# Optimization experiments

Hardware: AMD Instinct MI355X
Metric: run time of the kernel (lower is better)

## Reference

```python
import jax, jax.numpy as jnp
import numpy as np

N_NODES = 50000
N_EDGES = 1600000
N_GRAPHS = 64


def _gcn_conv(x, row, col, ew, W, b, n_nodes):
    # x: [N, Fin] -> [N, Fout]; PyG GCNConv: lin, add self-loops (w=1),
    # symmetric normalization, scatter-add at target (col), + bias.
    x = x @ W
    loop = jnp.arange(n_nodes, dtype=row.dtype)
    r = jnp.concatenate([row, loop])
    c = jnp.concatenate([col, loop])
    w = jnp.concatenate([ew, jnp.ones((n_nodes,), dtype=ew.dtype)])
    deg = jax.ops.segment_sum(w, c, num_segments=n_nodes)
    dinv = jnp.where(deg > 0, jax.lax.rsqrt(jnp.where(deg > 0, deg, 1.0)), 0.0)
    norm = dinv[r] * w * dinv[c]                      # [E+N]
    msg = x[r] * norm[:, None]                        # [E+N, Fout] (dominant traffic)
    out = jax.ops.segment_sum(msg, c, num_segments=n_nodes)
    return out + b


def setup_inputs() -> dict:
    key = jax.random.key(0)
    ks = jax.random.split(key, 12)
    x = jax.random.normal(ks[0], (N_NODES, 128), dtype=jnp.float32)
    edge_index = jax.random.randint(ks[1], (2, N_EDGES), 0, N_NODES, dtype=jnp.int32)
    edge_attr = jax.random.uniform(ks[2], (N_EDGES,), dtype=jnp.float32)
    batch = jnp.sort(jax.random.randint(ks[3], (N_NODES,), 0, N_GRAPHS, dtype=jnp.int32))
    glorot = lambda k, fi, fo: jax.random.normal(k, (fi, fo), jnp.float32) * np.sqrt(2.0 / (fi + fo))
    return {
        "x": x, "edge_index": edge_index, "edge_attr": edge_attr, "batch": batch,
        "W1": glorot(ks[4], 128, 128), "b1": jnp.zeros((128,), jnp.float32),
        "W2": glorot(ks[5], 128, 64), "b2": jnp.zeros((64,), jnp.float32),
        "fc1_W": glorot(ks[6], 64, 128), "fc1_b": jnp.zeros((128,), jnp.float32),
        "fc2_W": glorot(ks[7], 128, 2), "fc2_b": jnp.zeros((2,), jnp.float32),
    }


def reference(x, edge_index, edge_attr, batch, W1, b1, W2, b2, fc1_W, fc1_b, fc2_W, fc2_b):
    row, col = edge_index[0], edge_index[1]
    h = jax.nn.relu(_gcn_conv(x, row, col, edge_attr, W1, b1, N_NODES))
    x1 = jax.nn.relu(_gcn_conv(h, row, col, edge_attr, W2, b2, N_NODES))
    # global mean pool over batch ids
    sums = jax.ops.segment_sum(x1, batch, num_segments=N_GRAPHS)
    cnt = jax.ops.segment_sum(jnp.ones((N_NODES,), x1.dtype), batch, num_segments=N_GRAPHS)
    x2 = sums / jnp.maximum(cnt, 1.0)[:, None]        # [B, 64]
    # dropout is identity in eval mode
    h = jax.nn.relu(x2 @ fc1_W + fc1_b)
    logits = h @ fc2_W + fc2_b                        # [B, 2]
    return jax.nn.log_softmax(logits, axis=1)
```

## Files before the change

### kernel.cpp

```cpp
#include <hip/hip_runtime.h>
#include <hip/hip_bf16.h>


#define CAP 64
#define OVFCAP 8192
#define NRANGE 512
#define MAXNRP 2048
#define BSTR 68
#define KP 136
#define PARTNB 1024

typedef float v2f  __attribute__((ext_vector_type(2)));
typedef float f32x4 __attribute__((ext_vector_type(4)));
typedef short bf16x8 __attribute__((ext_vector_type(8)));

__device__ inline unsigned short f2bf(float f) {
    unsigned u = __float_as_uint(f);
    u += 0x7FFFu + ((u >> 16) & 1u);
    return (unsigned short)(u >> 16);
}
__device__ inline void fp8x4_to_f32(unsigned w, float* o) {
    v2f lo = __builtin_amdgcn_cvt_pk_f32_fp8((int)w, false);
    v2f hi = __builtin_amdgcn_cvt_pk_f32_fp8((int)w, true);
    o[0] = lo[0]; o[1] = lo[1]; o[2] = hi[0]; o[3] = hi[1];
}
__device__ inline unsigned f32x4_to_fp8(float a, float b, float c, float d) {
    int w = 0;
    w = __builtin_amdgcn_cvt_pk_fp8_f32(a, b, w, false);
    w = __builtin_amdgcn_cvt_pk_fp8_f32(c, d, w, true);
    return (unsigned)w;
}
__device__ inline float dinv_of(int ws) {
    return rsqrtf((float)ws * (1.0f / 32768.0f) + 1.0f);
}

__global__ void part_kernel(const int* __restrict__ rows, const int* __restrict__ cols,
                            const float* __restrict__ ew, int* __restrict__ rangeCnt,
                            uint2* __restrict__ rng, int E, int NR, int RSEG,
                            const float* __restrict__ W1, const float* __restrict__ W2,
                            unsigned short* __restrict__ wt1, unsigned short* __restrict__ wt2) {
    const int t = threadIdx.x;
    if (blockIdx.x >= PARTNB) {
        if (blockIdx.x == PARTNB) {
            for (int i = t; i < 128 * 128; i += 256) {
                int c = i >> 7, k = i & 127;
                wt1[c * KP + k] = f2bf(W1[k * 128 + c]);
            }
        } else {
            for (int i = t; i < 64 * 128; i += 256) {
                int c = i >> 7, k = i & 127;
                wt2[c * KP + k] = f2bf(W2[k * 64 + c]);
            }
        }
        return;
    }
    __shared__ int hc[NRANGE];
    const int CS = (E + PARTNB - 1) / PARTNB;
    const int e0 = blockIdx.x * CS, e1 = min(e0 + CS, E);
    for (int i = t; i < NRANGE; i += 256) hc[i] = 0;
    __syncthreads();
    for (int e = e0 + t; e < e1; e += 256) {
        int r = cols[e] / NR;
        atomicAdd(&hc[r], 1);
    }
    __syncthreads();
    for (int i = t; i < NRANGE; i += 256)
        hc[i] = atomicAdd(&rangeCnt[i], hc[i]);
    __syncthreads();
    for (int e = e0 + t; e < e1; e += 256) {
        int c = cols[e];
        int r = c / NR;
        int q = (int)(ew[e] * 32768.0f);
        if (q > 32767) q = 32767;
        unsigned rec = ((unsigned)rows[e] << 15) | (unsigned)q;
        int pos = atomicAdd(&hc[r], 1);
        if (pos < RSEG) rng[(size_t)r * RSEG + pos] = make_uint2((unsigned)c, rec);
    }
}

__global__ __launch_bounds__(512)
void place_kernel(const uint2* __restrict__ rng, const int* __restrict__ rangeCnt,
                  int* __restrict__ cnt, int* __restrict__ wsum,
                  unsigned* __restrict__ slot, int4* __restrict__ ovf,
                  int* __restrict__ ovfcnt, int NR, int RSEG, int N) {
    __shared__ int cur[MAXNRP];
    __shared__ int wsl[MAXNRP];
    const int r = blockIdx.x;
    const int t = threadIdx.x;
    const int n0 = r * NR;
    for (int n = t; n < NR; n += 512) { cur[n] = 0; wsl[n] = 0; }
    __syncthreads();
    const int M = min(rangeCnt[r], RSEG);
    const uint2* lst = rng + (size_t)r * RSEG;
    for (int k = t; k < M; k += 512) {
        uint2 u2 = lst[k];
        int cl = (int)u2.x - n0;
        int q = (int)(u2.y & 32767u);
        int pos = atomicAdd(&cur[cl], 1);
        atomicAdd(&wsl[cl], q);
        if (pos < CAP) {
            slot[(size_t)u2.x * CAP + pos] = u2.y;
        } else {
            int o = atomicAdd(ovfcnt, 1);
            if (o < OVFCAP)
                ovf[o] = make_int4((int)(u2.y >> 15), (int)u2.x, q, 0);
        }
    }
    __syncthreads();
    for (int n = t; n < NR; n += 512) {
        int gn = n0 + n;
        if (gn < N) { cnt[gn] = cur[n]; wsum[gn] = wsl[n]; }
    }
}

__global__ void place_simple_kernel(const int* __restrict__ rows, const int* __restrict__ cols,
                                    const float* __restrict__ ew, int* __restrict__ cnt,
                                    int* __restrict__ wsum,
                                    unsigned* __restrict__ slot, int4* __restrict__ ovf,
                                    int* __restrict__ ovfcnt, int E) {
    int e = blockIdx.x * 256 + threadIdx.x;
    if (e >= E) return;
    int r = rows[e], c = cols[e];
    int q = (int)(ew[e] * 32768.0f);
    if (q > 32767) q = 32767;
    int pos = atomicAdd(&cnt[c], 1);
    atomicAdd(&wsum[c], q);
    if (pos < CAP) {
        slot[(size_t)c * CAP + pos] = ((unsigned)r << 15) | (unsigned)q;
    } else {
        int o = atomicAdd(ovfcnt, 1);
        if (o < OVFCAP) ovf[o] = make_int4(r, c, q, 0);
    }
}

template <int BN, bool AF32>
__global__ __launch_bounds__(256)
void gemm_mfma_kernel(const void* __restrict__ Av, const unsigned short* __restrict__ wt,
                      const int* __restrict__ wsum, unsigned char* __restrict__ outf8,
                      int M) {
    constexpr int CT = BN / 16;
    constexpr int EPS = BN + 4;
    __shared__ unsigned short wl[BN * KP];
    __shared__ float ep[4][16 * EPS];
    const int t = threadIdx.x;
    for (int i = t; i < BN * KP / 8; i += 256)
        ((uint4*)wl)[i] = ((const uint4*)wt)[i];
    __syncthreads();
    const int w = t >> 6, lane = t & 63;
    const int n16 = lane & 15, q = lane >> 4;
    const int rowBase = blockIdx.x * 64 + w * 16;
    int arow = rowBase + n16; if (arow >= M) arow = M - 1;
    f32x4 acc[CT];
    #pragma unroll
    for (int ct = 0; ct < CT; ++ct) acc[ct] = (f32x4){0.f, 0.f, 0.f, 0.f};
    #pragma unroll
    for (int kt = 0; kt < 4; ++kt) {
        bf16x8 af;
        if (AF32) {
            const float* ap = (const float*)Av + (size_t)arow * 128 + kt * 32 + q * 8;
            float4 a0 = *(const float4*)ap;
            float4 a1 = *(const float4*)(ap + 4);
            af[0] = (short)f2bf(a0.x); af[1] = (short)f2bf(a0.y);
            af[2] = (short)f2bf(a0.z); af[3] = (short)f2bf(a0.w);
            af[4] = (short)f2bf(a1.x); af[5] = (short)f2bf(a1.y);
            af[6] = (short)f2bf(a1.z); af[7] = (short)f2bf(a1.w);
        } else {
            af = *(const bf16x8*)((const unsigned short*)Av + (size_t)arow * 128 + kt * 32 + q * 8);
        }
        #pragma unroll
        for (int ct = 0; ct < CT; ++ct) {
            bf16x8 bfr = *(const bf16x8*)&wl[(ct * 16 + n16) * KP + kt * 32 + q * 8];
            acc[ct] = __builtin_amdgcn_mfma_f32_16x16x32_bf16(af, bfr, acc[ct], 0, 0, 0);
        }
    }
    #pragma unroll
    for (int ct = 0; ct < CT; ++ct)
        #pragma unroll
        for (int r = 0; r < 4; ++r)
            ep[w][(q * 4 + r) * EPS + ct * 16 + n16] = acc[ct][r];
    __syncthreads();
    const int lr = lane & 15;
    const int cc = (lane >> 4) * (BN / 4);
    int grow = rowBase + lr;
    if (grow < M) {
        float s = dinv_of(wsum[grow]);
        const float* src = &ep[w][lr * EPS + cc];
        #pragma unroll
        for (int u = 0; u < BN / 64; ++u) {
            int col0 = cc + u * 16;
            int slice = col0 >> 6, cw = col0 & 63;
            unsigned w0 = f32x4_to_fp8(src[u*16+ 0]*s, src[u*16+ 1]*s, src[u*16+ 2]*s, src[u*16+ 3]*s);
            unsigned w1 = f32x4_to_fp8(src[u*16+ 4]*s, src[u*16+ 5]*s, src[u*16+ 6]*s, src[u*16+ 7]*s);
            unsigned w2 = f32x4_to_fp8(src[u*16+ 8]*s, src[u*16+ 9]*s, src[u*16+10]*s, src[u*16+11]*s);
            unsigned w3 = f32x4_to_fp8(src[u*16+12]*s, src[u*16+13]*s, src[u*16+14]*s, src[u*16+15]*s);
            *(uint4*)&outf8[((size_t)slice * M + grow) * 64 + cw] = make_uint4(w0, w1, w2, w3);
        }
    }
}

template <int F, int S, bool OB, bool POOL>
__global__ void gather_kernel(const unsigned char* __restrict__ xsb,
                              const unsigned* __restrict__ slot,
                              const int* __restrict__ cnt, const int* __restrict__ wsum,
                              const float* __restrict__ b, const int4* __restrict__ ovf,
                              const int* __restrict__ ovfcnt, void* __restrict__ outv, int N,
                              const int* __restrict__ gbatch, float* __restrict__ gsums,
                              float* __restrict__ gcnt) {
    constexpr int EPN = 4;
    __shared__ unsigned sbkt[16 * BSTR];
    __shared__ float x1s[16 * 68];
    __shared__ int gidl[16];
    const int slice = (S > 1) ? ((int)blockIdx.x % S) : 0;
    const int grp = (S > 1) ? ((int)blockIdx.x / S) : blockIdx.x;
    const int t = threadIdx.x;
    const int node0 = grp * 16;
    {
        int ndl = t >> 4, part = t & 15;
        int snode = node0 + ndl; if (snode >= N) snode = N - 1;
        int sc = cnt[snode]; if (sc > CAP) sc = CAP;
        if (part * 4 < sc)
            *(uint4*)&sbkt[ndl * BSTR + part * 4] =
                *(const uint4*)&slot[(size_t)snode * CAP + part * 4];
    }
    if constexpr (POOL) {
        if (t < 16) {
            int sn = node0 + t;
            gidl[t] = (sn < N) ? gbatch[sn] : -1;
        }
    }
    __syncthreads();
    const int w = t >> 6, lane = t & 63;
    const int cg = lane & 3;
    const int e  = (lane >> 2) & 3;
    const int nd = lane >> 4;
    const int ndl = w * 4 + nd;
    const int i = node0 + ndl;
    const bool iv = (i < N);
    const int ic = iv ? i : 0;
    const uint4* xs4 = (const uint4*)(xsb + (size_t)slice * N * 64);
    int mraw = iv ? cnt[ic] : 0;
    int m = mraw > CAP ? CAP : mraw;
    const unsigned* lb = &sbkt[ndl * BSTR];
    float acc[16] = {};
    int j = e;
    for (; j + EPN < m; j += 2 * EPN) {
        unsigned u0 = lb[j], u1 = lb[j + EPN];
        float c0 = (float)(u0 & 32767u), c1 = (float)(u1 & 32767u);
        uint4 a0 = xs4[(size_t)(u0 >> 15) * 4 + cg];
        uint4 a1 = xs4[(size_t)(u1 >> 15) * 4 + cg];
        float f0[16], f1[16];
        fp8x4_to_f32(a0.x, f0 + 0);  fp8x4_to_f32(a0.y, f0 + 4);
        fp8x4_to_f32(a0.z, f0 + 8);  fp8x4_to_f32(a0.w, f0 + 12);
        fp8x4_to_f32(a1.x, f1 + 0);  fp8x4_to_f32(a1.y, f1 + 4);
        fp8x4_to_f32(a1.z, f1 + 8);  fp8x4_to_f32(a1.w, f1 + 12);
        #pragma unroll
        for (int k = 0; k < 16; ++k) acc[k] += f0[k] * c0 + f1[k] * c1;
    }
    if (j < m) {
        unsigned u = lb[j];
        float c = (float)(u & 32767u);
        uint4 a = xs4[(size_t)(u >> 15) * 4 + cg];
        float f[16];
        fp8x4_to_f32(a.x, f + 0);  fp8x4_to_f32(a.y, f + 4);
        fp8x4_to_f32(a.z, f + 8);  fp8x4_to_f32(a.w, f + 12);
        #pragma unroll
        for (int k = 0; k < 16; ++k) acc[k] += f[k] * c;
    }
    if (mraw > CAP) {
        int oc = *ovfcnt; if (oc > OVFCAP) oc = OVFCAP;
        for (int k = e; k < oc; k += EPN) {
            int4 r4 = ovf[k];
            if (r4.y == i) {
                float c = (float)r4.z;
                uint4 a = xs4[(size_t)r4.x * 4 + cg];
                float f[16];
                fp8x4_to_f32(a.x, f + 0);  fp8x4_to_f32(a.y, f + 4);
                fp8x4_to_f32(a.z, f + 8);  fp8x4_to_f32(a.w, f + 12);
                #pragma unroll
                for (int kk = 0; kk < 16; ++kk) acc[kk] += f[kk] * c;
            }
        }
    }
    #pragma unroll
    for (int k = 0; k < 16; ++k) {
        acc[k] += __shfl_xor(acc[k], 4);
        acc[k] += __shfl_xor(acc[k], 8);
    }
    if (e == 0 && iv) {
        float d = dinv_of(wsum[i]);
        float sa = d * (1.0f / 32768.0f);
        uint4 sv = xs4[(size_t)i * 4 + cg];
        float sf[16];
        fp8x4_to_f32(sv.x, sf + 0);  fp8x4_to_f32(sv.y, sf + 4);
        fp8x4_to_f32(sv.z, sf + 8);  fp8x4_to_f32(sv.w, sf + 12);
        const float* bb = &b[slice * 64 + cg * 16];
        float o[16];
        #pragma unroll
        for (int k = 0; k < 16; ++k)
            o[k] = fmaxf(acc[k] * sa + sf[k] * d + bb[k], 0.f);
        if (OB) {
            unsigned short* dst = (unsigned short*)outv + (size_t)i * F + slice * 64 + cg * 16;
            unsigned pw[8];
            #pragma unroll
            for (int k = 0; k < 8; ++k)
                pw[k] = (unsigned)f2bf(o[2 * k]) | ((unsigned)f2bf(o[2 * k + 1]) << 16);
            *(uint4*)&dst[0] = make_uint4(pw[0], pw[1], pw[2], pw[3]);
            *(uint4*)&dst[8] = make_uint4(pw[4], pw[5], pw[6], pw[7]);
        } else if constexpr (!POOL) {
            float* dst = (float*)outv + (size_t)i * F + slice * 64 + cg * 16;
            *(float4*)&dst[0]  = make_float4(o[0], o[1], o[2], o[3]);
            *(float4*)&dst[4]  = make_float4(o[4], o[5], o[6], o[7]);
            *(float4*)&dst[8]  = make_float4(o[8], o[9], o[10], o[11]);
            *(float4*)&dst[12] = make_float4(o[12], o[13], o[14], o[15]);
        } else {
            float* dst = &x1s[ndl * 68 + cg * 16];
            *(float4*)&dst[0]  = make_float4(o[0], o[1], o[2], o[3]);
            *(float4*)&dst[4]  = make_float4(o[4], o[5], o[6], o[7]);
            *(float4*)&dst[8]  = make_float4(o[8], o[9], o[10], o[11]);
            *(float4*)&dst[12] = make_float4(o[12], o[13], o[14], o[15]);
        }
    }
    if constexpr (POOL) {
        __syncthreads();
        if (t < 64) {
            const int f = t;
            float run = 0.f; int gcur = -1;
            #pragma unroll 4
            for (int n = 0; n < 16; ++n) {
                int g = gidl[n];
                if (g < 0) break;
                if (g != gcur) {
                    if (gcur >= 0) atomicAdd(&gsums[gcur * 64 + f], run);
                    run = 0.f; gcur = g;
                }
                run += x1s[n * 68 + f];
            }
            if (gcur >= 0) atomicAdd(&gsums[gcur * 64 + f], run);
        } else if (t == 64) {
            float rc = 0.f; int gcur = -1;
            for (int n = 0; n < 16; ++n) {
                int g = gidl[n];
                if (g < 0) break;
                if (g != gcur) {
                    if (gcur >= 0) atomicAdd(&gcnt[gcur], rc);
                    rc = 0.f; gcur = g;
                }
                rc += 1.f;
            }
            if (gcur >= 0) atomicAdd(&gcnt[gcur], rc);
        }
    }
}

__global__ void head_kernel(const float* __restrict__ sums, const float* __restrict__ cnt,
                            const float* __restrict__ fc1W, const float* __restrict__ fc1b,
                            const float* __restrict__ fc2W, const float* __restrict__ fc2b,
                            float* __restrict__ out) {
    __shared__ float x2s[64];
    __shared__ float hs[128];
    __shared__ float lg[2];
    const int g = blockIdx.x;
    const int t = threadIdx.x;
    if (t < 64) {
        float c = fmaxf(cnt[g], 1.f);
        x2s[t] = sums[g * 64 + t] / c;
    }
    __syncthreads();
    {
        float a = fc1b[t];
        #pragma unroll 8
        for (int j = 0; j < 64; ++j) a += x2s[j] * fc1W[j * 128 + t];
        hs[t] = fmaxf(a, 0.f);
    }
    __syncthreads();
    {
        int m = t >> 6, l = t & 63;
        float p = hs[l] * fc2W[l * 2 + m] + hs[l + 64] * fc2W[(l + 64) * 2 + m];
        #pragma unroll
        for (int off = 1; off < 64; off <<= 1) p += __shfl_xor(p, off);
        if (l == 0) lg[m] = p + fc2b[m];
    }
    __syncthreads();
    if (t == 0) {
        float l0 = lg[0], l1 = lg[1];
        float mx = fmaxf(l0, l1);
        float lse = mx + logf(expf(l0 - mx) + expf(l1 - mx));
        out[g * 2 + 0] = l0 - lse;
        out[g * 2 + 1] = l1 - lse;
    }
}

extern "C" void kernel_launch(void* const* d_in, const int* in_sizes, int n_in,
                              void* d_out, int out_size, void* d_ws, size_t ws_size,
                              hipStream_t stream) {
    const float* x      = (const float*)d_in[0];
    const int*   eidx   = (const int*)d_in[1];
    const float* ew     = (const float*)d_in[2];
    const int*   batch  = (const int*)d_in[3];
    const float* W1     = (const float*)d_in[4];
    const float* b1     = (const float*)d_in[5];
    const float* W2     = (const float*)d_in[6];
    const float* b2     = (const float*)d_in[7];
    const float* fc1W   = (const float*)d_in[8];
    const float* fc1b   = (const float*)d_in[9];
    const float* fc2W   = (const float*)d_in[10];
    const float* fc2b   = (const float*)d_in[11];
    float* out = (float*)d_out;

    const int N = in_sizes[3];
    const int E = in_sizes[2];
    const int G = 64;
    const int* rows = eidx;
    const int* cols = eidx + E;
    const int NR = (N + NRANGE - 1) / NRANGE;
    const int RSEG = E / NRANGE + 2048;

    float* ws = (float*)d_ws;
    size_t off = 0;
    auto alloc = [&](size_t n) { float* p = ws + off; off += (n + 15) & ~(size_t)15; return p; };
    float*    sums     = alloc(64 * 64);
    float*    cntf     = alloc(16);
    int*      ovfcnt   = (int*)alloc(16);
    int*      rangeCnt = (int*)alloc(NRANGE);
    int*      cnt      = (int*)alloc(N);
    int*      wsum     = (int*)alloc(N);
    size_t zfloats = off;
    unsigned short* wt1 = (unsigned short*)alloc(128 * KP / 2 + 16);
    unsigned short* wt2 = (unsigned short*)alloc(64 * KP / 2 + 16);
    unsigned* slot   = (unsigned*)alloc((size_t)N * CAP);
    int4*     ovf    = (int4*)alloc((size_t)OVFCAP * 4);
    float*    bufA   = alloc((size_t)N * 128);
    float*    bufB   = alloc((size_t)N * 128);
    unsigned char*  xw1f8 = (unsigned char*)bufA;
    unsigned char*  xw2f8 = (unsigned char*)bufA;
    uint2*          rng   = (uint2*)bufB;
    unsigned short* hbf   = (unsigned short*)bufB;
    (void)ws_size;

    hipMemsetAsync(d_ws, 0, zfloats * sizeof(float), stream);

    const bool fits = (NR <= MAXNRP) &&
                      ((size_t)NRANGE * RSEG * sizeof(uint2) <= (size_t)N * 512);
    if (fits) {
        part_kernel<<<PARTNB + 2, 256, 0, stream>>>(rows, cols, ew, rangeCnt, rng, E, NR, RSEG,
                                                    W1, W2, wt1, wt2);
        place_kernel<<<NRANGE, 512, 0, stream>>>(rng, rangeCnt, cnt, wsum, slot, ovf, ovfcnt,
                                                 NR, RSEG, N);
    } else {
        part_kernel<<<PARTNB + 2, 256, 0, stream>>>(rows, cols, ew, rangeCnt, rng, 0, NR, RSEG,
                                                    W1, W2, wt1, wt2);
        place_simple_kernel<<<(E + 255) / 256, 256, 0, stream>>>(rows, cols, ew, cnt, wsum,
                                                                 slot, ovf, ovfcnt, E);
    }

    gemm_mfma_kernel<128, true><<<(N + 63) / 64, 256, 0, stream>>>(x, wt1, wsum, xw1f8, N);
    gather_kernel<128, 2, true, false><<<((N + 15) / 16) * 2, 256, 0, stream>>>(
        xw1f8, slot, cnt, wsum, b1, ovf, ovfcnt, hbf, N, nullptr, nullptr, nullptr);

    gemm_mfma_kernel<64, false><<<(N + 63) / 64, 256, 0, stream>>>(hbf, wt2, wsum, xw2f8, N);
    gather_kernel<64, 1, false, true><<<(N + 15) / 16, 256, 0, stream>>>(
        xw2f8, slot, cnt, wsum, b2, ovf, ovfcnt, nullptr, N, batch, sums, cntf);

    head_kernel<<<G, 128, 0, stream>>>(sums, cntf, fc1W, fc1b, fc2W, fc2b, out);
}
```

Baseline: 235.4 us.

## Stage partitioned edges in LDS before writing contiguous range segments

The edge partition kernel now uses 256 blocks of 512 threads. Each block buckets its chunk of edges in shared memory, using a block-wide exclusive scan over the 512 range counts, and then writes each bucket contiguously to its global range segment. The goal is to replace scattered 8-byte global writes with more coalesced runs and to cut global atomic contention. The cost is about 55KB of LDS per block, which limits occupancy, and a fallback path is kept for chunks larger than the buffer.

```diff
diff --git a/kernel.cpp b/kernel.cpp
--- a/kernel.cpp
+++ b/kernel.cpp
@@ -8,7 +8,8 @@
 #define MAXNRP 2048
 #define BSTR 68
 #define KP 136
-#define PARTNB 1024
+#define PARTNB 256
+#define PBUF 6400
 
 typedef float v2f  __attribute__((ext_vector_type(2)));
 typedef float f32x4 __attribute__((ext_vector_type(4)));
@@ -34,47 +35,95 @@
     return rsqrtf((float)ws * (1.0f / 32768.0f) + 1.0f);
 }
 
-__global__ void part_kernel(const int* __restrict__ rows, const int* __restrict__ cols,
-                            const float* __restrict__ ew, int* __restrict__ rangeCnt,
-                            uint2* __restrict__ rng, int E, int NR, int RSEG,
-                            const float* __restrict__ W1, const float* __restrict__ W2,
-                            unsigned short* __restrict__ wt1, unsigned short* __restrict__ wt2) {
+__global__ __launch_bounds__(512)
+void part_kernel(const int* __restrict__ rows, const int* __restrict__ cols,
+                 const float* __restrict__ ew, int* __restrict__ rangeCnt,
+                 uint2* __restrict__ rng, int E, int NR, int RSEG,
+                 const float* __restrict__ W1, const float* __restrict__ W2,
+                 unsigned short* __restrict__ wt1, unsigned short* __restrict__ wt2) {
     const int t = threadIdx.x;
     if (blockIdx.x >= PARTNB) {
         if (blockIdx.x == PARTNB) {
-            for (int i = t; i < 128 * 128; i += 256) {
+            for (int i = t; i < 128 * 128; i += 512) {
                 int c = i >> 7, k = i & 127;
                 wt1[c * KP + k] = f2bf(W1[k * 128 + c]);
             }
         } else {
-            for (int i = t; i < 64 * 128; i += 256) {
+            for (int i = t; i < 64 * 128; i += 512) {
                 int c = i >> 7, k = i & 127;
                 wt2[c * KP + k] = f2bf(W2[k * 64 + c]);
             }
         }
         return;
     }
-    __shared__ int hc[NRANGE];
+    __shared__ uint2 buf[PBUF];
+    __shared__ int hcnt[NRANGE];
+    __shared__ int lbase[NRANGE];
+    __shared__ int gbase[NRANGE];
+    __shared__ int wtot[8];
     const int CS = (E + PARTNB - 1) / PARTNB;
     const int e0 = blockIdx.x * CS, e1 = min(e0 + CS, E);
-    for (int i = t; i < NRANGE; i += 256) hc[i] = 0;
-    __syncthreads();
-    for (int e = e0 + t; e < e1; e += 256) {
-        int r = cols[e] / NR;
-        atomicAdd(&hc[r], 1);
-    }
-    __syncthreads();
-    for (int i = t; i < NRANGE; i += 256)
-        hc[i] = atomicAdd(&rangeCnt[i], hc[i]);
-    __syncthreads();
-    for (int e = e0 + t; e < e1; e += 256) {
-        int c = cols[e];
-        int r = c / NR;
-        int q = (int)(ew[e] * 32768.0f);
-        if (q > 32767) q = 32767;
-        unsigned rec = ((unsigned)rows[e] << 15) | (unsigned)q;
-        int pos = atomicAdd(&hc[r], 1);
-        if (pos < RSEG) rng[(size_t)r * RSEG + pos] = make_uint2((unsigned)c, rec);
+    const int M = e1 - e0;
+
+    if (CS <= PBUF) {
+        for (int i = t; i < NRANGE; i += 512) hcnt[i] = 0;
+        __syncthreads();
+        for (int e = e0 + t; e < e1; e += 512)
+            atomicAdd(&hcnt[cols[e] / NR], 1);
+        __syncthreads();
+        {
+            int v = hcnt[t];
+            int inc = v;
+            #pragma unroll
+            for (int off = 1; off < 64; off <<= 1) {
+                int n = __shfl_up(inc, off);
+                if ((t & 63) >= off) inc += n;
+            }
+            const int w = t >> 6;
+            if ((t & 63) == 63) wtot[w] = inc;
+            __syncthreads();
+            int wo = 0;
+            for (int k = 0; k < w; ++k) wo += wtot[k];
+            int excl = wo + inc - v;
+            lbase[t] = excl;
+            gbase[t] = (v > 0) ? atomicAdd(&rangeCnt[t], v) : 0;
+            hcnt[t] = excl;
+        }
+        __syncthreads();
+        for (int e = e0 + t; e < e1; e += 512) {
+            int c = cols[e];
+            int r = c / NR;
+            int q = (int)(ew[e] * 32768.0f);
+            if (q > 32767) q = 32767;
+            unsigned rec = ((unsigned)rows[e] << 15) | (unsigned)q;
+            int p = atomicAdd(&hcnt[r], 1);
+            buf[p] = make_uint2((unsigned)c, rec);
+        }
+        __syncthreads();
+        for (int i = t; i < M; i += 512) {
+            uint2 u = buf[i];
+            int r = (int)u.x / NR;
+            int idx = gbase[r] + (i - lbase[r]);
+            if (idx < RSEG) rng[(size_t)r * RSEG + idx] = u;
+        }
+    } else {
+        for (int i = t; i < NRANGE; i += 512) hcnt[i] = 0;
+        __syncthreads();
+        for (int e = e0 + t; e < e1; e += 512)
+            atomicAdd(&hcnt[cols[e] / NR], 1);
+        __syncthreads();
+        for (int i = t; i < NRANGE; i += 512)
+            hcnt[i] = atomicAdd(&rangeCnt[i], hcnt[i]);
+        __syncthreads();
+        for (int e = e0 + t; e < e1; e += 512) {
+            int c = cols[e];
+            int r = c / NR;
+            int q = (int)(ew[e] * 32768.0f);
+            if (q > 32767) q = 32767;
+            unsigned rec = ((unsigned)rows[e] << 15) | (unsigned)q;
+            int pos = atomicAdd(&hcnt[r], 1);
+            if (pos < RSEG) rng[(size_t)r * RSEG + pos] = make_uint2((unsigned)c, rec);
+        }
     }
 }
 
@@ -442,12 +491,12 @@
     const bool fits = (NR <= MAXNRP) &&
                       ((size_t)NRANGE * RSEG * sizeof(uint2) <= (size_t)N * 512);
     if (fits) {
-        part_kernel<<<PARTNB + 2, 256, 0, stream>>>(rows, cols, ew, rangeCnt, rng, E, NR, RSEG,
+        part_kernel<<<PARTNB + 2, 512, 0, stream>>>(rows, cols, ew, rangeCnt, rng, E, NR, RSEG,
                                                     W1, W2, wt1, wt2);
         place_kernel<<<NRANGE, 512, 0, stream>>>(rng, rangeCnt, cnt, wsum, slot, ovf, ovfcnt,
                                                  NR, RSEG, N);
     } else {
-        part_kernel<<<PARTNB + 2, 256, 0, stream>>>(rows, cols, ew, rangeCnt, rng, 0, NR, RSEG,
+        part_kernel<<<PARTNB + 2, 512, 0, stream>>>(rows, cols, ew, rangeCnt, rng, 0, NR, RSEG,
                                                     W1, W2, wt1, wt2);
         place_simple_kernel<<<(E + 255) / 256, 256, 0, stream>>>(rows, cols, ew, cnt, wsum,
                                                                  slot, ovf, ovfcnt, E);
```

Result: faster. 213.9 us (-9.1%).
